# Kernel tuning notes

Hardware: AMD Instinct MI355X
Metric: run time of the kernel (lower is better)

## Reference

```python
import jax, jax.numpy as jnp
import numpy as np

H = 1024          # hid_dim
SEQ = 149         # input tokens (cls makes 150)
B = 128           # batch
WIN = 20          # local attention band half-width (hard-coded in module)


def _pe_table(n, d):
    # ConstantPE with period=1: position = 2*pi*arange(n)
    pos = 2.0 * np.pi * np.arange(n, dtype=np.float64)[:, None]
    div = np.exp(np.arange(0, d, 2, dtype=np.float64) * (-np.log(10000.0) / d))
    pe = np.zeros((n, d), dtype=np.float32)
    pe[:, 0::2] = np.sin(pos * div)
    pe[:, 1::2] = np.cos(pos * div)
    return jnp.asarray(pe)


def _band_mask(n, w=WIN):
    # True where attention is DISALLOWED (matches src_mask == 1)
    r = np.arange(n)[:, None]
    c = np.arange(n)[None, :]
    allowed = (c >= np.maximum(r - w, 0)) & (c < r + w)
    allowed[0, :] = True  # cls row attends everywhere
    return jnp.asarray(~allowed)


def _layer_norm(x, g, b, eps=1e-5):
    m = jnp.mean(x, axis=-1, keepdims=True)
    v = jnp.var(x, axis=-1, keepdims=True)
    return (x - m) * jax.lax.rsqrt(v + eps) * g + b


def setup_inputs() -> dict:
    key = jax.random.key(0)
    ks = jax.random.split(key, 8)
    s = 0.02
    return {
        "z": jax.random.normal(ks[0], (SEQ, B, H), jnp.float32),
        "cls_token": jax.random.normal(ks[1], (1, H), jnp.float32),
        "ln_g": jnp.ones((H,), jnp.float32),
        "ln_b": jnp.zeros((H,), jnp.float32),
        "w_qkv": jax.random.normal(ks[2], (H, 3 * H), jnp.float32) * s,
        "b_qkv": jnp.zeros((3 * H,), jnp.float32),
        "w_o": jax.random.normal(ks[3], (H, H), jnp.float32) * s,
        "b_o": jnp.zeros((H,), jnp.float32),
        "w_m1": jax.random.normal(ks[4], (H, H), jnp.float32) * s,
        "b_m1": jnp.zeros((H,), jnp.float32),
        "w_m2": jax.random.normal(ks[5], (H, H), jnp.float32) * s,
        "b_m2": jnp.zeros((H,), jnp.float32),
    }


def reference(z, cls_token, ln_g, ln_b, w_qkv, b_qkv, w_o, b_o, w_m1, b_m1, w_m2, b_m2):
    S1 = z.shape[0] + 1  # tokens incl. cls
    pe = _pe_table(S1, H)          # (S1, H)
    neg_mask = _band_mask(S1)      # (S1, S1) bool, True = masked

    x = jnp.swapaxes(z, 0, 1)                                   # (B, S, H)
    cls = jnp.broadcast_to(cls_token[None], (x.shape[0], 1, H))  # (B, 1, H)
    x = jnp.concatenate([cls, x], axis=1)                        # (B, S1, H)
    x = _layer_norm(x + pe[None], ln_g, ln_b)

    qkv = x @ w_qkv + b_qkv
    q, k, v = jnp.split(qkv, 3, axis=-1)

    attn = jnp.einsum("bqh,bkh->bqk", q, k) / jnp.sqrt(jnp.float32(H))
    attn = jnp.where(neg_mask[None], jnp.float32(-1e10), attn)
    attn = jax.nn.softmax(attn, axis=-1)

    sa = jnp.einsum("bqk,bkh->bqh", attn, v) @ w_o + b_o
    zsa = _layer_norm(x + sa, ln_g, ln_b)

    mlp = jax.nn.gelu(zsa @ w_m1 + b_m1, approximate=False) @ w_m2 + b_m2
    out = zsa + mlp
    return jnp.swapaxes(out, 0, 1)  # (S1, B, H)
```

## Files before the change

kernel.cpp:

```cpp
#include <hip/hip_runtime.h>
#include <math.h>

#define HD 1024
#define S1 150
#define BATCH 128
#define MTOK (S1 * BATCH)
#define WIN 20
#define QKVLD (3 * HD)

typedef unsigned short bf16_t;
typedef short s16x8 __attribute__((ext_vector_type(8)));
typedef float f32x4 __attribute__((ext_vector_type(4)));

__device__ __forceinline__ float bf2f(unsigned int u16) {
  return __uint_as_float(u16 << 16);
}
__device__ __forceinline__ unsigned short f2bf(float f) {
  unsigned int u = __float_as_uint(f);
  u += 0x7fff + ((u >> 16) & 1);
  return (unsigned short)(u >> 16);
}

__device__ __forceinline__ float wave_sum(float v) {
#pragma unroll
  for (int o = 32; o; o >>= 1) v += __shfl_down(v, o, 64);
  return v;
}

__device__ __forceinline__ void gload_lds16(const bf16_t* g, bf16_t* l) {
  __builtin_amdgcn_global_load_lds(
      (const __attribute__((address_space(1))) unsigned int*)(unsigned long long)(const void*)g,
      (__attribute__((address_space(3))) unsigned int*)(unsigned int)(unsigned long long)(void*)l,
      16, 0, 0);
}

__global__ __launch_bounds__(256) void transpose_kernel(
    const float* __restrict__ W, bf16_t* __restrict__ WT, int K, int N) {
  __shared__ float t[32][33];
  int n0 = blockIdx.x * 32, k0 = blockIdx.y * 32;
  int tx = threadIdx.x, ty = threadIdx.y;
#pragma unroll
  for (int i = 0; i < 4; i++)
    t[ty + i * 8][tx] = W[(size_t)(k0 + ty + i * 8) * N + n0 + tx];
  __syncthreads();
#pragma unroll
  for (int i = 0; i < 4; i++)
    WT[(size_t)(n0 + ty + i * 8) * K + k0 + tx] = f2bf(t[tx][ty + i * 8]);
}

__global__ void pe_kernel(float* __restrict__ pe) {
  int s = blockIdx.x;
  double pos = 6.283185307179586476925286766559 * (double)s;
  for (int p = threadIdx.x; p < HD / 2; p += blockDim.x) {
    double dv = exp((double)(2 * p) * (-9.210340371976184 / (double)HD));
    double a = pos * dv;
    pe[s * HD + 2 * p] = (float)sin(a);
    pe[s * HD + 2 * p + 1] = (float)cos(a);
  }
}

__global__ __launch_bounds__(256) void build_x_kernel(
    const float* __restrict__ z, const float* __restrict__ cls,
    const float* __restrict__ pe, const float* __restrict__ g,
    const float* __restrict__ be, bf16_t* __restrict__ x) {
  int t = blockIdx.x;
  int b = t / S1, s = t % S1;
  const float* src = (s == 0) ? cls : (z + ((size_t)(s - 1) * BATCH + b) * HD);
  const float* pr = pe + (size_t)s * HD;
  int tid = threadIdx.x;
  float vals[4];
  float sum = 0.f, sq = 0.f;
#pragma unroll
  for (int i = 0; i < 4; i++) {
    int h = tid + i * 256;
    float v = src[h] + pr[h];
    vals[i] = v;
    sum += v;
    sq += v * v;
  }
  __shared__ float shs[4], shq[4];
  __shared__ float sm, sr;
  sum = wave_sum(sum);
  sq = wave_sum(sq);
  int wave = tid >> 6, lane = tid & 63;
  if (!lane) { shs[wave] = sum; shq[wave] = sq; }
  __syncthreads();
  if (!tid) {
    float S = shs[0] + shs[1] + shs[2] + shs[3];
    float Q = shq[0] + shq[1] + shq[2] + shq[3];
    float mean = S * (1.f / HD);
    float var = Q * (1.f / HD) - mean * mean;
    sm = mean;
    sr = rsqrtf(var + 1e-5f);
  }
  __syncthreads();
  float mean = sm, rstd = sr;
  bf16_t* xr = x + (size_t)t * HD;
#pragma unroll
  for (int i = 0; i < 4; i++) {
    int h = tid + i * 256;
    xr[h] = f2bf((vals[i] - mean) * rstd * g[h] + be[h]);
  }
}

__global__ __launch_bounds__(256) void ln_residual_kernel(
    const bf16_t* __restrict__ a, const bf16_t* __restrict__ r,
    const float* __restrict__ g, const float* __restrict__ be,
    bf16_t* __restrict__ out) {
  int t = blockIdx.x;
  int tid = threadIdx.x;
  const bf16_t* ar = a + (size_t)t * QKVLD;
  const bf16_t* rr = r + (size_t)t * HD;
  float vals[4];
  float sum = 0.f, sq = 0.f;
#pragma unroll
  for (int i = 0; i < 4; i++) {
    int h = tid + i * 256;
    float v = bf2f(ar[h]) + bf2f(rr[h]);
    vals[i] = v;
    sum += v;
    sq += v * v;
  }
  __shared__ float shs[4], shq[4];
  __shared__ float sm, sr;
  sum = wave_sum(sum);
  sq = wave_sum(sq);
  int wave = tid >> 6, lane = tid & 63;
  if (!lane) { shs[wave] = sum; shq[wave] = sq; }
  __syncthreads();
  if (!tid) {
    float S = shs[0] + shs[1] + shs[2] + shs[3];
    float Q = shq[0] + shq[1] + shq[2] + shq[3];
    float mean = S * (1.f / HD);
    float var = Q * (1.f / HD) - mean * mean;
    sm = mean;
    sr = rsqrtf(var + 1e-5f);
  }
  __syncthreads();
  float mean = sm, rstd = sr;
  bf16_t* outp = out + (size_t)t * QKVLD;
#pragma unroll
  for (int i = 0; i < 4; i++) {
    int h = tid + i * 256;
    outp[h] = f2bf((vals[i] - mean) * rstd * g[h] + be[h]);
  }
}

template <int EPI>
__global__ __launch_bounds__(256) void mfma_gemm_kernel(
    const bf16_t* __restrict__ A, int lda, const bf16_t* __restrict__ WT,
    const float* __restrict__ bias, bf16_t* __restrict__ C, int ldc, int N) {
  constexpr int K = 1024;
  __shared__ bf16_t As[128 * 32];
  __shared__ bf16_t Bs[128 * 32];
  int tid = threadIdx.x;
  int w = tid >> 6, lane = tid & 63;
  int wm = w >> 1, wn = w & 1;
  int m0 = blockIdx.y * 128, n0 = blockIdx.x * 128;

  int srow = lane >> 2;
  int scol = ((lane & 3) ^ ((lane >> 3) & 3)) * 8;
  const bf16_t* gA0 = A + (size_t)(m0 + w * 32 + srow) * lda + scol;
  const bf16_t* gA1 = gA0 + (size_t)16 * lda;
  const bf16_t* gB0 = WT + (size_t)(n0 + w * 32 + srow) * K + scol;
  const bf16_t* gB1 = gB0 + (size_t)16 * K;
  bf16_t* lA0 = As + (w * 32) * 32;
  bf16_t* lA1 = As + (w * 32 + 16) * 32;
  bf16_t* lB0 = Bs + (w * 32) * 32;
  bf16_t* lB1 = Bs + (w * 32 + 16) * 32;

  int frow = lane & 15;
  int slot = (lane >> 4) ^ ((frow >> 1) & 3);
  int aoff[4], boff[4];
#pragma unroll
  for (int t = 0; t < 4; t++) {
    aoff[t] = (wm * 64 + t * 16 + frow) * 32 + slot * 8;
    boff[t] = (wn * 64 + t * 16 + frow) * 32 + slot * 8;
  }

  f32x4 acc[4][4] = {};

  for (int k0 = 0; k0 < K; k0 += 32) {
    gload_lds16(gA0, lA0);
    gload_lds16(gA1, lA1);
    gload_lds16(gB0, lB0);
    gload_lds16(gB1, lB1);
    gA0 += 32; gA1 += 32; gB0 += 32; gB1 += 32;
    __syncthreads();
    s16x8 af[4], bf[4];
#pragma unroll
    for (int t = 0; t < 4; t++) {
      af[t] = *(const s16x8*)(As + aoff[t]);
      bf[t] = *(const s16x8*)(Bs + boff[t]);
    }
#pragma unroll
    for (int i = 0; i < 4; i++)
#pragma unroll
      for (int j = 0; j < 4; j++)
        acc[i][j] = __builtin_amdgcn_mfma_f32_16x16x32_bf16(af[i], bf[j], acc[i][j], 0, 0, 0);
    __syncthreads();
  }

  int erow = (lane >> 4) * 4, ecol = lane & 15;
#pragma unroll
  for (int j = 0; j < 4; j++) {
    int n = n0 + wn * 64 + j * 16 + ecol;
    float bb = bias[n];
#pragma unroll
    for (int i = 0; i < 4; i++) {
      int mb = m0 + wm * 64 + i * 16 + erow;
#pragma unroll
      for (int r = 0; r < 4; r++) {
        float v = acc[i][j][r] + bb;
        if (EPI == 1) v = 0.5f * v * (1.f + erff(v * 0.7071067811865476f));
        C[(size_t)(mb + r) * ldc + n] = f2bf(v);
      }
    }
  }
}

__global__ __launch_bounds__(256) void mfma_gemm_out_kernel(
    const bf16_t* __restrict__ A, int lda, const bf16_t* __restrict__ WT,
    const float* __restrict__ bias, const bf16_t* __restrict__ res,
    float* __restrict__ out) {
  constexpr int K = 1024;
  __shared__ bf16_t As[128 * 32];
  __shared__ bf16_t Bs[128 * 32];
  int tid = threadIdx.x;
  int w = tid >> 6, lane = tid & 63;
  int wm = w >> 1, wn = w & 1;
  int m0 = blockIdx.y * 128, n0 = blockIdx.x * 128;

  int srow = lane >> 2;
  int scol = ((lane & 3) ^ ((lane >> 3) & 3)) * 8;
  const bf16_t* gA0 = A + (size_t)(m0 + w * 32 + srow) * lda + scol;
  const bf16_t* gA1 = gA0 + (size_t)16 * lda;
  const bf16_t* gB0 = WT + (size_t)(n0 + w * 32 + srow) * K + scol;
  const bf16_t* gB1 = gB0 + (size_t)16 * K;
  bf16_t* lA0 = As + (w * 32) * 32;
  bf16_t* lA1 = As + (w * 32 + 16) * 32;
  bf16_t* lB0 = Bs + (w * 32) * 32;
  bf16_t* lB1 = Bs + (w * 32 + 16) * 32;

  int frow = lane & 15;
  int slot = (lane >> 4) ^ ((frow >> 1) & 3);
  int aoff[4], boff[4];
#pragma unroll
  for (int t = 0; t < 4; t++) {
    aoff[t] = (wm * 64 + t * 16 + frow) * 32 + slot * 8;
    boff[t] = (wn * 64 + t * 16 + frow) * 32 + slot * 8;
  }

  f32x4 acc[4][4] = {};

  for (int k0 = 0; k0 < K; k0 += 32) {
    gload_lds16(gA0, lA0);
    gload_lds16(gA1, lA1);
    gload_lds16(gB0, lB0);
    gload_lds16(gB1, lB1);
    gA0 += 32; gA1 += 32; gB0 += 32; gB1 += 32;
    __syncthreads();
    s16x8 af[4], bf[4];
#pragma unroll
    for (int t = 0; t < 4; t++) {
      af[t] = *(const s16x8*)(As + aoff[t]);
      bf[t] = *(const s16x8*)(Bs + boff[t]);
    }
#pragma unroll
    for (int i = 0; i < 4; i++)
#pragma unroll
      for (int j = 0; j < 4; j++)
        acc[i][j] = __builtin_amdgcn_mfma_f32_16x16x32_bf16(af[i], bf[j], acc[i][j], 0, 0, 0);
    __syncthreads();
  }

  int erow = (lane >> 4) * 4, ecol = lane & 15;
#pragma unroll
  for (int j = 0; j < 4; j++) {
    int n = n0 + wn * 64 + j * 16 + ecol;
    float bb = bias[n];
#pragma unroll
    for (int i = 0; i < 4; i++) {
      int mb = m0 + wm * 64 + i * 16 + erow;
#pragma unroll
      for (int r = 0; r < 4; r++) {
        int m = mb + r;
        int b = m / S1, s = m % S1;
        float v = acc[i][j][r] + bb + bf2f(res[(size_t)m * QKVLD + n]);
        out[((size_t)s * BATCH + b) * HD + n] = v;
      }
    }
  }
}

__global__ __launch_bounds__(256) void attn_tile_kernel(bf16_t* __restrict__ qkv) {
  int g = blockIdx.x;
  int xcd = g & 7, tt0 = g >> 3;
  int qt = tt0 % 5, b = xcd + 8 * (tt0 / 5);
  int q0 = qt * 32;

  int lo_col = (qt == 0) ? 0 : (q0 - 20);
  int hi_col = (qt == 0) ? 150 : ((q0 + 51 < 150) ? q0 + 51 : 150);
  int ct0 = lo_col >> 5;
  int cth = (hi_col + 31) >> 5;
  int NCT = cth - ct0;
  int W = NCT * 32;
  int NSUB = NCT * 2;
  int NT = 2 * NSUB;
  int T = NT >> 2;

  __shared__ bf16_t Qs[2 * 32 * 32];
  __shared__ bf16_t Ks[2 * 160 * 32];
  __shared__ float S[32][164];

  int tid = threadIdx.x;
  int w = tid >> 6, lane = tid & 63;

  const bf16_t* kvbase = qkv + (size_t)b * S1 * QKVLD;

  int sr = lane >> 2;
  int scol = ((lane & 3) ^ ((lane >> 3) & 3)) * 8;
  int frow = lane & 15;
  int fslot = (((lane >> 4) ^ ((frow >> 1) & 3))) * 8;

  f32x4 acc[5] = {};

  int U1 = 2 + NSUB;

  for (int k0 = 0; k0 < 1024; k0 += 64) {
    for (int uu = w; uu < 2 * U1; uu += 4) {
      int p = (uu >= U1) ? 1 : 0;
      int ur = uu - p * U1;
      int col = k0 + p * 32 + scol;
      if (ur < 2) {
        int qrow = q0 + ur * 16 + sr;
        if (qrow > 149) qrow = 149;
        gload_lds16(kvbase + (size_t)qrow * QKVLD + col,
                    Qs + p * 1024 + (ur * 16) * 32);
      } else {
        int cr0 = (ur - 2) * 16;
        int cg = ct0 * 32 + cr0 + sr;
        if (cg > 149) cg = 149;
        gload_lds16(kvbase + (size_t)cg * QKVLD + HD + col,
                    Ks + p * 5120 + cr0 * 32);
      }
    }
    __syncthreads();
    s16x8 af0[2], af1[2];
#pragma unroll
    for (int p = 0; p < 2; p++) {
      af0[p] = *(const s16x8*)(Qs + p * 1024 + (0 * 16 + frow) * 32 + fslot);
      af1[p] = *(const s16x8*)(Qs + p * 1024 + (1 * 16 + frow) * 32 + fslot);
    }
#pragma unroll
    for (int t = 0; t < 5; t++) {
      if (t < T) {
        int tidt = w + t * 4;
        int qs = (tidt >= NSUB) ? 1 : 0;
        int cs = tidt - qs * NSUB;
#pragma unroll
        for (int p = 0; p < 2; p++) {
          s16x8 bf = *(const s16x8*)(Ks + p * 5120 + (cs * 16 + frow) * 32 + fslot);
          s16x8 a = qs ? af1[p] : af0[p];
          acc[t] = __builtin_amdgcn_mfma_f32_16x16x32_bf16(a, bf, acc[t], 0, 0, 0);
        }
      }
    }
    __syncthreads();
  }

  int erow = (lane >> 4) * 4, ecol = lane & 15;
#pragma unroll
  for (int t = 0; t < 5; t++) {
    if (t < T) {
      int tidt = w + t * 4;
      int qs = (tidt >= NSUB) ? 1 : 0;
      int cs = tidt - qs * NSUB;
#pragma unroll
      for (int r = 0; r < 4; r++) {
        int qrel = qs * 16 + erow + r;
        int crel = cs * 16 + ecol;
        int qg = q0 + qrel, cg = ct0 * 32 + crel;
        bool ok = (qg < 150) && (cg < 150) &&
                  ((qg == 0) || (cg >= qg - WIN && cg < qg + WIN));
        S[qrel][crel] = ok ? acc[t][r] * 0.03125f : -1e30f;
      }
    }
  }
  __syncthreads();

  {
    int q = tid >> 3, j = tid & 7;
    float m = -1e30f;
    for (int c = j; c < W; c += 8) m = fmaxf(m, S[q][c]);
#pragma unroll
    for (int o = 1; o < 8; o <<= 1) m = fmaxf(m, __shfl_xor(m, o, 64));
    float s = 0.f;
    for (int c = j; c < W; c += 8) {
      float e = __expf(S[q][c] - m);
      S[q][c] = e;
      s += e;
    }
#pragma unroll
    for (int o = 1; o < 8; o <<= 1) s += __shfl_xor(s, o, 64);
    float inv = 1.f / s;
    for (int c = j; c < W; c += 8) S[q][c] *= inv;
  }
  __syncthreads();

  int qg0 = q0 + 8 * w;
  if (qg0 < 150) {
    int lo = (qt == 0 && w == 0) ? 0 : ((qg0 - WIN > 0) ? qg0 - WIN : 0);
    int hi = (qt == 0 && w == 0) ? 150 : ((qg0 + 27 < 150) ? qg0 + 27 : 150);
    int c0base = ct0 * 32;
#pragma unroll
    for (int hp = 0; hp < 2; hp++) {
      int hb = hp * 512 + lane * 8;
      float a[8][8];
#pragma unroll
      for (int qi = 0; qi < 8; qi++)
#pragma unroll
        for (int e = 0; e < 8; e++) a[qi][e] = 0.f;
      const bf16_t* vb = kvbase + 2 * HD + hb;
      for (int c = lo; c < hi; ++c) {
        uint4 vv = *(const uint4*)(vb + (size_t)c * QKVLD);
        float vf[8];
        vf[0] = __uint_as_float(vv.x << 16);
        vf[1] = __uint_as_float(vv.x & 0xffff0000u);
        vf[2] = __uint_as_float(vv.y << 16);
        vf[3] = __uint_as_float(vv.y & 0xffff0000u);
        vf[4] = __uint_as_float(vv.z << 16);
        vf[5] = __uint_as_float(vv.z & 0xffff0000u);
        vf[6] = __uint_as_float(vv.w << 16);
        vf[7] = __uint_as_float(vv.w & 0xffff0000u);
        int crel = c - c0base;
#pragma unroll
        for (int qi = 0; qi < 8; qi++) {
          float p = S[8 * w + qi][crel];
#pragma unroll
          for (int e = 0; e < 8; e++) a[qi][e] += p * vf[e];
        }
      }
#pragma unroll
      for (int qi = 0; qi < 8; qi++) {
        int qg = qg0 + qi;
        if (qg < 150) {
          uint4 pk;
          pk.x = (unsigned int)f2bf(a[qi][0]) | ((unsigned int)f2bf(a[qi][1]) << 16);
          pk.y = (unsigned int)f2bf(a[qi][2]) | ((unsigned int)f2bf(a[qi][3]) << 16);
          pk.z = (unsigned int)f2bf(a[qi][4]) | ((unsigned int)f2bf(a[qi][5]) << 16);
          pk.w = (unsigned int)f2bf(a[qi][6]) | ((unsigned int)f2bf(a[qi][7]) << 16);
          *(uint4*)(qkv + ((size_t)b * S1 + qg) * QKVLD + hb) = pk;
        }
      }
    }
  }
}

extern "C" void kernel_launch(void* const* d_in, const int* in_sizes, int n_in,
                              void* d_out, int out_size, void* d_ws, size_t ws_size,
                              hipStream_t stream) {
  (void)in_sizes; (void)n_in; (void)out_size; (void)ws_size;
  const float* z = (const float*)d_in[0];
  const float* cls = (const float*)d_in[1];
  const float* ln_g = (const float*)d_in[2];
  const float* ln_b = (const float*)d_in[3];
  const float* w_qkv = (const float*)d_in[4];
  const float* b_qkv = (const float*)d_in[5];
  const float* w_o = (const float*)d_in[6];
  const float* b_o = (const float*)d_in[7];
  const float* w_m1 = (const float*)d_in[8];
  const float* b_m1 = (const float*)d_in[9];
  const float* w_m2 = (const float*)d_in[10];
  const float* b_m2 = (const float*)d_in[11];

  char* wsb = (char*)d_ws;
  bf16_t* wt_m2 = (bf16_t*)wsb;
  float* pe = (float*)(wsb + 2097152);
  bf16_t* qkv = (bf16_t*)(wsb + 2097152 + 614400);

  char* outb = (char*)d_out;
  bf16_t* x = (bf16_t*)outb;
  bf16_t* wt_qkv = (bf16_t*)(outb + 39321600);
  bf16_t* wt_o = (bf16_t*)(outb + 45613056);
  bf16_t* wt_m1 = (bf16_t*)(outb + 47710208);

  bf16_t* av = qkv;
  bf16_t* sa = qkv + HD;
  bf16_t* zsa = qkv + 2 * HD;
  bf16_t* h1 = qkv;
  float* out = (float*)d_out;

  transpose_kernel<<<dim3(96, 32), dim3(32, 8), 0, stream>>>(w_qkv, wt_qkv, HD, 3 * HD);
  transpose_kernel<<<dim3(32, 32), dim3(32, 8), 0, stream>>>(w_o, wt_o, HD, HD);
  transpose_kernel<<<dim3(32, 32), dim3(32, 8), 0, stream>>>(w_m1, wt_m1, HD, HD);
  transpose_kernel<<<dim3(32, 32), dim3(32, 8), 0, stream>>>(w_m2, wt_m2, HD, HD);
  pe_kernel<<<S1, 256, 0, stream>>>(pe);
  build_x_kernel<<<MTOK, 256, 0, stream>>>(z, cls, pe, ln_g, ln_b, x);
  mfma_gemm_kernel<0><<<dim3(24, 150), 256, 0, stream>>>(
      x, HD, wt_qkv, b_qkv, qkv, QKVLD, 3 * HD);
  attn_tile_kernel<<<640, 256, 0, stream>>>(qkv);
  mfma_gemm_kernel<0><<<dim3(8, 150), 256, 0, stream>>>(
      av, QKVLD, wt_o, b_o, sa, QKVLD, HD);
  ln_residual_kernel<<<MTOK, 256, 0, stream>>>(sa, x, ln_g, ln_b, zsa);
  mfma_gemm_kernel<1><<<dim3(8, 150), 256, 0, stream>>>(
      zsa, QKVLD, wt_m1, b_m1, h1, QKVLD, HD);
  mfma_gemm_out_kernel<<<dim3(8, 150), 256, 0, stream>>>(
      h1, QKVLD, wt_m2, b_m2, zsa, out);
}
```

Baseline: 707.3 us.

## Replace GEMMs with 256x256-tile, 4-stage pipelined MFMA kernel

Replaces the 128x128 single-buffered MFMA GEMMs with one templated 256x256-tile kernel using 512 threads and a 4-deep LDS ring buffer. Global-to-LDS loads are prefetched three k-steps ahead with vmcnt waits and one barrier per step. A and B prefetches are interleaved with MFMA bursts under raised wave priority. The output GEMM is folded in as an epilogue variant. The aim is to hide load latency, raise arithmetic intensity per tile, and halve barrier counts. The cost is much larger LDS use (128KB per block) and more registers, with fewer blocks per CU and a coarser grid (75 row tiles). The 256-row tiles divide 19200 evenly.

```diff
diff --git a/kernel.cpp b/kernel.cpp
--- a/kernel.cpp
+++ b/kernel.cpp
@@ -147,59 +147,86 @@
 }
 
 template <int EPI>
-__global__ __launch_bounds__(256) void mfma_gemm_kernel(
+__global__ __launch_bounds__(512, 2) void gemm256_kernel(
     const bf16_t* __restrict__ A, int lda, const bf16_t* __restrict__ WT,
-    const float* __restrict__ bias, bf16_t* __restrict__ C, int ldc, int N) {
-  constexpr int K = 1024;
-  __shared__ bf16_t As[128 * 32];
-  __shared__ bf16_t Bs[128 * 32];
+    const float* __restrict__ bias, bf16_t* __restrict__ C, int ldc,
+    const bf16_t* __restrict__ res, float* __restrict__ outf) {
+  constexpr int NT = 32;
+  __shared__ bf16_t ALDS[4 * 8192];
+  __shared__ bf16_t BLDS[4 * 8192];
   int tid = threadIdx.x;
   int w = tid >> 6, lane = tid & 63;
-  int wm = w >> 1, wn = w & 1;
-  int m0 = blockIdx.y * 128, n0 = blockIdx.x * 128;
-
-  int srow = lane >> 2;
-  int scol = ((lane & 3) ^ ((lane >> 3) & 3)) * 8;
-  const bf16_t* gA0 = A + (size_t)(m0 + w * 32 + srow) * lda + scol;
-  const bf16_t* gA1 = gA0 + (size_t)16 * lda;
-  const bf16_t* gB0 = WT + (size_t)(n0 + w * 32 + srow) * K + scol;
-  const bf16_t* gB1 = gB0 + (size_t)16 * K;
-  bf16_t* lA0 = As + (w * 32) * 32;
-  bf16_t* lA1 = As + (w * 32 + 16) * 32;
-  bf16_t* lB0 = Bs + (w * 32) * 32;
-  bf16_t* lB1 = Bs + (w * 32 + 16) * 32;
+  int wm = w >> 2, wn = w & 3;
+  int m0 = blockIdx.y * 256, n0 = blockIdx.x * 256;
+
+  int sr = lane >> 2;
+  int scol = ((lane & 3) ^ ((sr >> 1) & 3)) * 8;
+  const bf16_t* gA = A + (size_t)(m0 + w * 16 + sr) * lda + scol;
+  const bf16_t* gB = WT + (size_t)(n0 + w * 16 + sr) * 1024 + scol;
+  bf16_t* lA = ALDS + w * 512;
+  bf16_t* lB = BLDS + w * 512;
+  size_t ldh = (size_t)128 * lda;
+
+#define STAGE_A(tt)                                                   \
+  do {                                                                \
+    int bb_ = (tt) & 3;                                               \
+    gload_lds16(gA + (tt) * 32, lA + bb_ * 8192);                     \
+    gload_lds16(gA + ldh + (tt) * 32, lA + bb_ * 8192 + 4096);        \
+  } while (0)
+#define STAGE_B(tt)                                                   \
+  do {                                                                \
+    int bb_ = (tt) & 3;                                               \
+    gload_lds16(gB + (tt) * 32, lB + bb_ * 8192);                     \
+    gload_lds16(gB + 131072 + (tt) * 32, lB + bb_ * 8192 + 4096);     \
+  } while (0)
 
   int frow = lane & 15;
-  int slot = (lane >> 4) ^ ((frow >> 1) & 3);
-  int aoff[4], boff[4];
-#pragma unroll
-  for (int t = 0; t < 4; t++) {
-    aoff[t] = (wm * 64 + t * 16 + frow) * 32 + slot * 8;
-    boff[t] = (wn * 64 + t * 16 + frow) * 32 + slot * 8;
-  }
-
-  f32x4 acc[4][4] = {};
-
-  for (int k0 = 0; k0 < K; k0 += 32) {
-    gload_lds16(gA0, lA0);
-    gload_lds16(gA1, lA1);
-    gload_lds16(gB0, lB0);
-    gload_lds16(gB1, lB1);
-    gA0 += 32; gA1 += 32; gB0 += 32; gB1 += 32;
-    __syncthreads();
-    s16x8 af[4], bf[4];
-#pragma unroll
-    for (int t = 0; t < 4; t++) {
-      af[t] = *(const s16x8*)(As + aoff[t]);
-      bf[t] = *(const s16x8*)(Bs + boff[t]);
-    }
-#pragma unroll
-    for (int i = 0; i < 4; i++)
-#pragma unroll
-      for (int j = 0; j < 4; j++)
-        acc[i][j] = __builtin_amdgcn_mfma_f32_16x16x32_bf16(af[i], bf[j], acc[i][j], 0, 0, 0);
-    __syncthreads();
-  }
+  int fslot = ((lane >> 4) ^ ((frow >> 1) & 3)) * 8;
+  int aoff[8], boff[4];
+#pragma unroll
+  for (int i = 0; i < 8; i++) aoff[i] = (wm * 8 + i) * 512 + frow * 32 + fslot;
+#pragma unroll
+  for (int j = 0; j < 4; j++) boff[j] = (wn * 4 + j) * 512 + frow * 32 + fslot;
+
+  f32x4 acc[8][4] = {};
+
+  STAGE_A(0); STAGE_B(0);
+  STAGE_A(1); STAGE_B(1);
+  STAGE_A(2); STAGE_B(2);
+
+  for (int t = 0; t < NT; ++t) {
+    const bf16_t* Ab = ALDS + (t & 3) * 8192;
+    const bf16_t* Bb = BLDS + (t & 3) * 8192;
+    asm volatile("s_waitcnt vmcnt(8)" ::: "memory");
+    __builtin_amdgcn_s_barrier();
+    asm volatile("" ::: "memory");
+    bool pf = (t + 3 < NT);
+    if (pf) STAGE_A(t + 3);
+    s16x8 af[8], b0, b1;
+#pragma unroll
+    for (int i = 0; i < 8; i++) af[i] = *(const s16x8*)(Ab + aoff[i]);
+    b0 = *(const s16x8*)(Bb + boff[0]);
+    b1 = *(const s16x8*)(Bb + boff[1]);
+    __builtin_amdgcn_s_setprio(1);
+#pragma unroll
+    for (int i = 0; i < 8; i++) {
+      acc[i][0] = __builtin_amdgcn_mfma_f32_16x16x32_bf16(af[i], b0, acc[i][0], 0, 0, 0);
+      acc[i][1] = __builtin_amdgcn_mfma_f32_16x16x32_bf16(af[i], b1, acc[i][1], 0, 0, 0);
+    }
+    __builtin_amdgcn_s_setprio(0);
+    if (pf) STAGE_B(t + 3);
+    b0 = *(const s16x8*)(Bb + boff[2]);
+    b1 = *(const s16x8*)(Bb + boff[3]);
+    __builtin_amdgcn_s_setprio(1);
+#pragma unroll
+    for (int i = 0; i < 8; i++) {
+      acc[i][2] = __builtin_amdgcn_mfma_f32_16x16x32_bf16(af[i], b0, acc[i][2], 0, 0, 0);
+      acc[i][3] = __builtin_amdgcn_mfma_f32_16x16x32_bf16(af[i], b1, acc[i][3], 0, 0, 0);
+    }
+    __builtin_amdgcn_s_setprio(0);
+  }
+#undef STAGE_A
+#undef STAGE_B
 
   int erow = (lane >> 4) * 4, ecol = lane & 15;
 #pragma unroll
@@ -207,87 +234,20 @@
     int n = n0 + wn * 64 + j * 16 + ecol;
     float bb = bias[n];
 #pragma unroll
-    for (int i = 0; i < 4; i++) {
-      int mb = m0 + wm * 64 + i * 16 + erow;
+    for (int i = 0; i < 8; i++) {
+      int mb = m0 + wm * 128 + i * 16 + erow;
 #pragma unroll
       for (int r = 0; r < 4; r++) {
+        int m = mb + r;
         float v = acc[i][j][r] + bb;
         if (EPI == 1) v = 0.5f * v * (1.f + erff(v * 0.7071067811865476f));
-        C[(size_t)(mb + r) * ldc + n] = f2bf(v);
-      }
-    }
-  }
-}
-
-__global__ __launch_bounds__(256) void mfma_gemm_out_kernel(
-    const bf16_t* __restrict__ A, int lda, const bf16_t* __restrict__ WT,
-    const float* __restrict__ bias, const bf16_t* __restrict__ res,
-    float* __restrict__ out) {
-  constexpr int K = 1024;
-  __shared__ bf16_t As[128 * 32];
-  __shared__ bf16_t Bs[128 * 32];
-  int tid = threadIdx.x;
-  int w = tid >> 6, lane = tid & 63;
-  int wm = w >> 1, wn = w & 1;
-  int m0 = blockIdx.y * 128, n0 = blockIdx.x * 128;
-
-  int srow = lane >> 2;
-  int scol = ((lane & 3) ^ ((lane >> 3) & 3)) * 8;
-  const bf16_t* gA0 = A + (size_t)(m0 + w * 32 + srow) * lda + scol;
-  const bf16_t* gA1 = gA0 + (size_t)16 * lda;
-  const bf16_t* gB0 = WT + (size_t)(n0 + w * 32 + srow) * K + scol;
-  const bf16_t* gB1 = gB0 + (size_t)16 * K;
-  bf16_t* lA0 = As + (w * 32) * 32;
-  bf16_t* lA1 = As + (w * 32 + 16) * 32;
-  bf16_t* lB0 = Bs + (w * 32) * 32;
-  bf16_t* lB1 = Bs + (w * 32 + 16) * 32;
-
-  int frow = lane & 15;
-  int slot = (lane >> 4) ^ ((frow >> 1) & 3);
-  int aoff[4], boff[4];
-#pragma unroll
-  for (int t = 0; t < 4; t++) {
-    aoff[t] = (wm * 64 + t * 16 + frow) * 32 + slot * 8;
-    boff[t] = (wn * 64 + t * 16 + frow) * 32 + slot * 8;
-  }
-
-  f32x4 acc[4][4] = {};
-
-  for (int k0 = 0; k0 < K; k0 += 32) {
-    gload_lds16(gA0, lA0);
-    gload_lds16(gA1, lA1);
-    gload_lds16(gB0, lB0);
-    gload_lds16(gB1, lB1);
-    gA0 += 32; gA1 += 32; gB0 += 32; gB1 += 32;
-    __syncthreads();
-    s16x8 af[4], bf[4];
-#pragma unroll
-    for (int t = 0; t < 4; t++) {
-      af[t] = *(const s16x8*)(As + aoff[t]);
-      bf[t] = *(const s16x8*)(Bs + boff[t]);
-    }
-#pragma unroll
-    for (int i = 0; i < 4; i++)
-#pragma unroll
-      for (int j = 0; j < 4; j++)
-        acc[i][j] = __builtin_amdgcn_mfma_f32_16x16x32_bf16(af[i], bf[j], acc[i][j], 0, 0, 0);
-    __syncthreads();
-  }
-
-  int erow = (lane >> 4) * 4, ecol = lane & 15;
-#pragma unroll
-  for (int j = 0; j < 4; j++) {
-    int n = n0 + wn * 64 + j * 16 + ecol;
-    float bb = bias[n];
-#pragma unroll
-    for (int i = 0; i < 4; i++) {
-      int mb = m0 + wm * 64 + i * 16 + erow;
-#pragma unroll
-      for (int r = 0; r < 4; r++) {
-        int m = mb + r;
-        int b = m / S1, s = m % S1;
-        float v = acc[i][j][r] + bb + bf2f(res[(size_t)m * QKVLD + n]);
-        out[((size_t)s * BATCH + b) * HD + n] = v;
+        if (EPI == 2) {
+          int b = m / S1, s = m % S1;
+          v += bf2f(res[(size_t)m * QKVLD + n]);
+          outf[((size_t)s * BATCH + b) * HD + n] = v;
+        } else {
+          C[(size_t)m * ldc + n] = f2bf(v);
+        }
       }
     }
   }
@@ -497,14 +457,14 @@
   transpose_kernel<<<dim3(32, 32), dim3(32, 8), 0, stream>>>(w_m2, wt_m2, HD, HD);
   pe_kernel<<<S1, 256, 0, stream>>>(pe);
   build_x_kernel<<<MTOK, 256, 0, stream>>>(z, cls, pe, ln_g, ln_b, x);
-  mfma_gemm_kernel<0><<<dim3(24, 150), 256, 0, stream>>>(
-      x, HD, wt_qkv, b_qkv, qkv, QKVLD, 3 * HD);
+  gemm256_kernel<0><<<dim3(12, 75), 512, 0, stream>>>(
+      x, HD, wt_qkv, b_qkv, qkv, QKVLD, nullptr, nullptr);
   attn_tile_kernel<<<640, 256, 0, stream>>>(qkv);
-  mfma_gemm_kernel<0><<<dim3(8, 150), 256, 0, stream>>>(
-      av, QKVLD, wt_o, b_o, sa, QKVLD, HD);
+  gemm256_kernel<0><<<dim3(4, 75), 512, 0, stream>>>(
+      av, QKVLD, wt_o, b_o, sa, QKVLD, nullptr, nullptr);
   ln_residual_kernel<<<MTOK, 256, 0, stream>>>(sa, x, ln_g, ln_b, zsa);
-  mfma_gemm_kernel<1><<<dim3(8, 150), 256, 0, stream>>>(
-      zsa, QKVLD, wt_m1, b_m1, h1, QKVLD, HD);
-  mfma_gemm_out_kernel<<<dim3(8, 150), 256, 0, stream>>>(
-      h1, QKVLD, wt_m2, b_m2, zsa, out);
-}
+  gemm256_kernel<1><<<dim3(4, 75), 512, 0, stream>>>(
+      zsa, QKVLD, wt_m1, b_m1, h1, QKVLD, nullptr, nullptr);
+  gemm256_kernel<2><<<dim3(4, 75), 512, 0, stream>>>(
+      h1, QKVLD, wt_m2, b_m2, nullptr, 0, zsa, out);
+}
```

Measured after the change: 743.9 us. +5.2%, slower.

## Double GEMM K-step to 64, merge weight transposes, unify output GEMM template

Applied to the files above, without the earlier changes.

The MFMA GEMM now loads two 32-wide K slices per iteration into doubled LDS buffers, which halves the number of barrier pairs per K loop at the cost of twice the LDS per block. The four weight-transpose launches are merged into one kernel that picks its matrix from the block index, removing launch overhead. The separate output GEMM kernel becomes an EPI==2 specialisation of the shared template, which is mostly a cleanup. Higher LDS use may lower occupancy.

```diff
diff --git a/kernel.cpp b/kernel.cpp
--- a/kernel.cpp
+++ b/kernel.cpp
@@ -34,10 +34,27 @@
       16, 0, 0);
 }
 
-__global__ __launch_bounds__(256) void transpose_kernel(
-    const float* __restrict__ W, bf16_t* __restrict__ WT, int K, int N) {
+__global__ __launch_bounds__(256) void transpose_all_kernel(
+    const float* __restrict__ w_qkv, bf16_t* __restrict__ wt_qkv,
+    const float* __restrict__ w_o, bf16_t* __restrict__ wt_o,
+    const float* __restrict__ w_m1, bf16_t* __restrict__ wt_m1,
+    const float* __restrict__ w_m2, bf16_t* __restrict__ wt_m2) {
+  int g = blockIdx.x;
+  const float* W;
+  bf16_t* WT;
+  int N, bx, by;
+  if (g < 3072) {
+    W = w_qkv; WT = wt_qkv; N = 3072;
+    bx = g % 96; by = g / 96;
+  } else {
+    int r = g - 3072;
+    int which = r >> 10, l = r & 1023;
+    bx = l & 31; by = l >> 5; N = 1024;
+    W = (which == 0) ? w_o : (which == 1) ? w_m1 : w_m2;
+    WT = (which == 0) ? wt_o : (which == 1) ? wt_m1 : wt_m2;
+  }
   __shared__ float t[32][33];
-  int n0 = blockIdx.x * 32, k0 = blockIdx.y * 32;
+  int n0 = bx * 32, k0 = by * 32;
   int tx = threadIdx.x, ty = threadIdx.y;
 #pragma unroll
   for (int i = 0; i < 4; i++)
@@ -45,7 +62,7 @@
   __syncthreads();
 #pragma unroll
   for (int i = 0; i < 4; i++)
-    WT[(size_t)(n0 + ty + i * 8) * K + k0 + tx] = f2bf(t[tx][ty + i * 8]);
+    WT[(size_t)(n0 + ty + i * 8) * 1024 + k0 + tx] = f2bf(t[tx][ty + i * 8]);
 }
 
 __global__ void pe_kernel(float* __restrict__ pe) {
@@ -149,10 +166,11 @@
 template <int EPI>
 __global__ __launch_bounds__(256) void mfma_gemm_kernel(
     const bf16_t* __restrict__ A, int lda, const bf16_t* __restrict__ WT,
-    const float* __restrict__ bias, bf16_t* __restrict__ C, int ldc, int N) {
+    const float* __restrict__ bias, bf16_t* __restrict__ C, int ldc,
+    const bf16_t* __restrict__ res, float* __restrict__ outf) {
   constexpr int K = 1024;
-  __shared__ bf16_t As[128 * 32];
-  __shared__ bf16_t Bs[128 * 32];
+  __shared__ bf16_t As[2 * 128 * 32];
+  __shared__ bf16_t Bs[2 * 128 * 32];
   int tid = threadIdx.x;
   int w = tid >> 6, lane = tid & 63;
   int wm = w >> 1, wn = w & 1;
@@ -180,24 +198,31 @@
 
   f32x4 acc[4][4] = {};
 
-  for (int k0 = 0; k0 < K; k0 += 32) {
+  for (int k0 = 0; k0 < K; k0 += 64) {
     gload_lds16(gA0, lA0);
     gload_lds16(gA1, lA1);
     gload_lds16(gB0, lB0);
     gload_lds16(gB1, lB1);
-    gA0 += 32; gA1 += 32; gB0 += 32; gB1 += 32;
+    gload_lds16(gA0 + 32, lA0 + 4096);
+    gload_lds16(gA1 + 32, lA1 + 4096);
+    gload_lds16(gB0 + 32, lB0 + 4096);
+    gload_lds16(gB1 + 32, lB1 + 4096);
+    gA0 += 64; gA1 += 64; gB0 += 64; gB1 += 64;
     __syncthreads();
-    s16x8 af[4], bf[4];
-#pragma unroll
-    for (int t = 0; t < 4; t++) {
-      af[t] = *(const s16x8*)(As + aoff[t]);
-      bf[t] = *(const s16x8*)(Bs + boff[t]);
-    }
-#pragma unroll
-    for (int i = 0; i < 4; i++)
-#pragma unroll
-      for (int j = 0; j < 4; j++)
-        acc[i][j] = __builtin_amdgcn_mfma_f32_16x16x32_bf16(af[i], bf[j], acc[i][j], 0, 0, 0);
+#pragma unroll
+    for (int p = 0; p < 2; p++) {
+      s16x8 af[4], bf[4];
+#pragma unroll
+      for (int t = 0; t < 4; t++) {
+        af[t] = *(const s16x8*)(As + p * 4096 + aoff[t]);
+        bf[t] = *(const s16x8*)(Bs + p * 4096 + boff[t]);
+      }
+#pragma unroll
+      for (int i = 0; i < 4; i++)
+#pragma unroll
+        for (int j = 0; j < 4; j++)
+          acc[i][j] = __builtin_amdgcn_mfma_f32_16x16x32_bf16(af[i], bf[j], acc[i][j], 0, 0, 0);
+    }
     __syncthreads();
   }
 
@@ -211,83 +236,16 @@
       int mb = m0 + wm * 64 + i * 16 + erow;
 #pragma unroll
       for (int r = 0; r < 4; r++) {
+        int m = mb + r;
         float v = acc[i][j][r] + bb;
         if (EPI == 1) v = 0.5f * v * (1.f + erff(v * 0.7071067811865476f));
-        C[(size_t)(mb + r) * ldc + n] = f2bf(v);
-      }
-    }
-  }
-}
-
-__global__ __launch_bounds__(256) void mfma_gemm_out_kernel(
-    const bf16_t* __restrict__ A, int lda, const bf16_t* __restrict__ WT,
-    const float* __restrict__ bias, const bf16_t* __restrict__ res,
-    float* __restrict__ out) {
-  constexpr int K = 1024;
-  __shared__ bf16_t As[128 * 32];
-  __shared__ bf16_t Bs[128 * 32];
-  int tid = threadIdx.x;
-  int w = tid >> 6, lane = tid & 63;
-  int wm = w >> 1, wn = w & 1;
-  int m0 = blockIdx.y * 128, n0 = blockIdx.x * 128;
-
-  int srow = lane >> 2;
-  int scol = ((lane & 3) ^ ((lane >> 3) & 3)) * 8;
-  const bf16_t* gA0 = A + (size_t)(m0 + w * 32 + srow) * lda + scol;
-  const bf16_t* gA1 = gA0 + (size_t)16 * lda;
-  const bf16_t* gB0 = WT + (size_t)(n0 + w * 32 + srow) * K + scol;
-  const bf16_t* gB1 = gB0 + (size_t)16 * K;
-  bf16_t* lA0 = As + (w * 32) * 32;
-  bf16_t* lA1 = As + (w * 32 + 16) * 32;
-  bf16_t* lB0 = Bs + (w * 32) * 32;
-  bf16_t* lB1 = Bs + (w * 32 + 16) * 32;
-
-  int frow = lane & 15;
-  int slot = (lane >> 4) ^ ((frow >> 1) & 3);
-  int aoff[4], boff[4];
-#pragma unroll
-  for (int t = 0; t < 4; t++) {
-    aoff[t] = (wm * 64 + t * 16 + frow) * 32 + slot * 8;
-    boff[t] = (wn * 64 + t * 16 + frow) * 32 + slot * 8;
-  }
-
-  f32x4 acc[4][4] = {};
-
-  for (int k0 = 0; k0 < K; k0 += 32) {
-    gload_lds16(gA0, lA0);
-    gload_lds16(gA1, lA1);
-    gload_lds16(gB0, lB0);
-    gload_lds16(gB1, lB1);
-    gA0 += 32; gA1 += 32; gB0 += 32; gB1 += 32;
-    __syncthreads();
-    s16x8 af[4], bf[4];
-#pragma unroll
-    for (int t = 0; t < 4; t++) {
-      af[t] = *(const s16x8*)(As + aoff[t]);
-      bf[t] = *(const s16x8*)(Bs + boff[t]);
-    }
-#pragma unroll
-    for (int i = 0; i < 4; i++)
-#pragma unroll
-      for (int j = 0; j < 4; j++)
-        acc[i][j] = __builtin_amdgcn_mfma_f32_16x16x32_bf16(af[i], bf[j], acc[i][j], 0, 0, 0);
-    __syncthreads();
-  }
-
-  int erow = (lane >> 4) * 4, ecol = lane & 15;
-#pragma unroll
-  for (int j = 0; j < 4; j++) {
-    int n = n0 + wn * 64 + j * 16 + ecol;
-    float bb = bias[n];
-#pragma unroll
-    for (int i = 0; i < 4; i++) {
-      int mb = m0 + wm * 64 + i * 16 + erow;
-#pragma unroll
-      for (int r = 0; r < 4; r++) {
-        int m = mb + r;
-        int b = m / S1, s = m % S1;
-        float v = acc[i][j][r] + bb + bf2f(res[(size_t)m * QKVLD + n]);
-        out[((size_t)s * BATCH + b) * HD + n] = v;
+        if (EPI == 2) {
+          int b = m / S1, s = m % S1;
+          v += bf2f(res[(size_t)m * QKVLD + n]);
+          outf[((size_t)s * BATCH + b) * HD + n] = v;
+        } else {
+          C[(size_t)m * ldc + n] = f2bf(v);
+        }
       }
     }
   }
@@ -491,20 +449,18 @@
   bf16_t* h1 = qkv;
   float* out = (float*)d_out;
 
-  transpose_kernel<<<dim3(96, 32), dim3(32, 8), 0, stream>>>(w_qkv, wt_qkv, HD, 3 * HD);
-  transpose_kernel<<<dim3(32, 32), dim3(32, 8), 0, stream>>>(w_o, wt_o, HD, HD);
-  transpose_kernel<<<dim3(32, 32), dim3(32, 8), 0, stream>>>(w_m1, wt_m1, HD, HD);
-  transpose_kernel<<<dim3(32, 32), dim3(32, 8), 0, stream>>>(w_m2, wt_m2, HD, HD);
+  transpose_all_kernel<<<6144, dim3(32, 8), 0, stream>>>(
+      w_qkv, wt_qkv, w_o, wt_o, w_m1, wt_m1, w_m2, wt_m2);
   pe_kernel<<<S1, 256, 0, stream>>>(pe);
   build_x_kernel<<<MTOK, 256, 0, stream>>>(z, cls, pe, ln_g, ln_b, x);
   mfma_gemm_kernel<0><<<dim3(24, 150), 256, 0, stream>>>(
-      x, HD, wt_qkv, b_qkv, qkv, QKVLD, 3 * HD);
+      x, HD, wt_qkv, b_qkv, qkv, QKVLD, nullptr, nullptr);
   attn_tile_kernel<<<640, 256, 0, stream>>>(qkv);
   mfma_gemm_kernel<0><<<dim3(8, 150), 256, 0, stream>>>(
-      av, QKVLD, wt_o, b_o, sa, QKVLD, HD);
+      av, QKVLD, wt_o, b_o, sa, QKVLD, nullptr, nullptr);
   ln_residual_kernel<<<MTOK, 256, 0, stream>>>(sa, x, ln_g, ln_b, zsa);
   mfma_gemm_kernel<1><<<dim3(8, 150), 256, 0, stream>>>(
-      zsa, QKVLD, wt_m1, b_m1, h1, QKVLD, HD);
-  mfma_gemm_out_kernel<<<dim3(8, 150), 256, 0, stream>>>(
-      h1, QKVLD, wt_m2, b_m2, zsa, out);
-}
+      zsa, QKVLD, wt_m1, b_m1, h1, QKVLD, nullptr, nullptr);
+  mfma_gemm_kernel<2><<<dim3(8, 150), 256, 0, stream>>>(
+      h1, QKVLD, wt_m2, b_m2, nullptr, 0, zsa, out);
+}
```

After: 695.5 us. About the same (-1.7%).
